# Optimization experiments

Measured on AMD Instinct MI355X. Metric: run time of the kernel, lower is better.

Reference implementation:

```python
import jax, jax.numpy as jnp
import numpy as np

N_RAYS = 131072
N_NODES = 524288
ENC_DEPTH = 8
ENC_DIM = 16
N_POINTS = 8
IN_DIM = N_POINTS * ENC_DEPTH * ENC_DIM  # 1024
INNER = 64


def setup_inputs() -> dict:
    key = jax.random.key(0)
    ks = jax.random.split(key, 9)
    orig = jax.random.uniform(ks[0], (N_RAYS, 3), dtype=jnp.float32)
    end = jax.random.uniform(ks[1], (N_RAYS, 3), dtype=jnp.float32)
    history = jax.random.randint(ks[2], (N_RAYS, ENC_DEPTH), 0, N_NODES, dtype=jnp.int32).astype(jnp.int64)
    nodes_min = jax.random.uniform(ks[3], (N_NODES, 3), dtype=jnp.float32)
    # extents strictly positive (module replaces 0 extents with 0.5)
    nodes_extent = jax.random.uniform(ks[4], (N_NODES, 3), dtype=jnp.float32) + 0.1
    emb = jax.random.normal(ks[5], (N_NODES, 8 * ENC_DIM), dtype=jnp.float32) * 0.1
    W1 = jax.random.normal(ks[6], (IN_DIM, INNER), dtype=jnp.float32) * (1.0 / np.sqrt(IN_DIM))
    W2 = jax.random.normal(ks[7], (INNER, INNER), dtype=jnp.float32) * (1.0 / np.sqrt(INNER))
    W3 = jax.random.normal(ks[8], (INNER, 2), dtype=jnp.float32) * (1.0 / np.sqrt(INNER))
    return {"orig": orig, "end": end, "history": history, "nodes_min": nodes_min,
            "nodes_extent": nodes_extent, "emb": emb, "W1": W1, "W2": W2, "W3": W3}


def _net_forward(orig, end, history, nodes_min, nodes_extent, emb, W1, W2, W3):
    n = orig.shape[0]
    d = history.shape[1]
    # gather per-ray, per-depth node data (irregular access)
    nmin = nodes_min[history]          # (n, d, 3)
    ext = nodes_extent[history]        # (n, d, 3)
    po = jnp.clip((orig[:, None, :] - nmin) / ext, 0.0, 1.0)  # (n, d, 3)
    pe = jnp.clip((end[:, None, :] - nmin) / ext, 0.0, 1.0)
    ts = jnp.linspace(0.0, 1.0, N_POINTS, dtype=orig.dtype)
    pts = po[:, :, None, :] + (pe - po)[:, :, None, :] * ts[None, None, :, None]  # (n, d, P, 3)
    xd, yd, zd = pts[..., 0], pts[..., 1], pts[..., 2]
    # corner weights in the same order as bbox_feature.chunk(8): 000,100,010,001,101,011,110,111
    w = jnp.stack([
        (1 - xd) * (1 - yd) * (1 - zd),
        xd * (1 - yd) * (1 - zd),
        (1 - xd) * yd * (1 - zd),
        (1 - xd) * (1 - yd) * zd,
        xd * (1 - yd) * zd,
        (1 - xd) * yd * zd,
        xd * yd * (1 - zd),
        xd * yd * zd,
    ], axis=-1)                                    # (n, d, P, 8)
    corners = emb[history].reshape(n, d, 8, ENC_DIM)  # (n, d, 8, F)
    feat = jnp.einsum('ndpk,ndkf->ndpf', w, corners)  # (n, d, P, F)
    feat = feat.reshape(n, d * N_POINTS * ENC_DIM)    # concat over depth
    h = jax.nn.relu(feat @ W1)
    h = jax.nn.relu(h @ W2)
    a = h @ W3                                        # (n, 2)
    lengths = jnp.linalg.norm(end - orig, axis=-1)
    pred_cls = a[:, 0]
    pred_dist = a[:, 1] * lengths
    return jnp.stack([pred_cls, pred_dist], axis=-1)  # (n, 2)


def reference(orig, end, history, nodes_min, nodes_extent, emb, W1, W2, W3):
    return _net_forward(orig, end, history, nodes_min, nodes_extent, emb, W1, W2, W3)
```

## Files before the change

### kernel.cpp

```cpp
#include <hip/hip_runtime.h>
#include <hip/hip_bf16.h>
#include <cstdint>

#define ENC_DEPTH 8
#define RAYS_PER_BLOCK 64
#define THREADS 512

typedef __attribute__((ext_vector_type(8))) short bf16x8;
typedef __attribute__((ext_vector_type(4))) float f32x4;

__device__ __forceinline__ unsigned short f2bf(float x) {
    union { float f; unsigned u; } v; v.f = x;
    unsigned r = v.u + 0x7fffu + ((v.u >> 16) & 1u);
    return (unsigned short)(r >> 16);
}
__device__ __forceinline__ float bf2f(unsigned short h) {
    union { unsigned u; float f; } v; v.u = ((unsigned)h) << 16;
    return v.f;
}
__device__ __forceinline__ float clamp01(float x) {
    return fminf(fmaxf(x, 0.0f), 1.0f);
}

__global__ __launch_bounds__(THREADS, 4) void nbvh_kernel(
    const float* __restrict__ orig, const float* __restrict__ endp,
    const int* __restrict__ hist, const float* __restrict__ nodes_min,
    const float* __restrict__ nodes_extent, const float* __restrict__ emb,
    const float* __restrict__ W1, const float* __restrict__ W2,
    const float* __restrict__ W3, float* __restrict__ out)
{
    __shared__ int hist_s[RAYS_PER_BLOCK * ENC_DEPTH];
    __shared__ float oe_s[RAYS_PER_BLOCK * 6];
    __shared__ __align__(16) unsigned short corners_s[RAYS_PER_BLOCK * 136];
    __shared__ __align__(16) unsigned short feat_s[RAYS_PER_BLOCK * 144];
    __shared__ __align__(16) unsigned short w1t_s[64 * 144];
    __shared__ float h1_s[RAYS_PER_BLOCK * 65];

    const int t = threadIdx.x;
    const int r0 = blockIdx.x * RAYS_PER_BLOCK;
    const int wave = t >> 6;
    const int lane = t & 63;

    hist_s[t] = hist[r0 * ENC_DEPTH + t];
    if (t < RAYS_PER_BLOCK * 3) {
        int ray = t / 3, c = t - ray * 3;
        oe_s[ray * 6 + c]     = orig[(r0 + ray) * 3 + c];
        oe_s[ray * 6 + 3 + c] = endp[(r0 + ray) * 3 + c];
    }

    f32x4 acc0 = {0.f, 0.f, 0.f, 0.f};
    f32x4 acc1 = {0.f, 0.f, 0.f, 0.f};
    const int m0 = (wave >> 1) * 16;
    const int n0 = (wave & 1) * 32;

    __syncthreads();

    for (int d = 0; d < ENC_DEPTH; ++d) {
        {
            int ray = t >> 3, k = t & 7;
            int node = hist_s[(ray << 3) + d];
            const float4* ep = (const float4*)(emb + ((size_t)node << 7) + (k << 4));
            float4 e0 = ep[0], e1 = ep[1], e2 = ep[2], e3 = ep[3];
            float e[16];
            e[0]=e0.x; e[1]=e0.y; e[2]=e0.z; e[3]=e0.w;
            e[4]=e1.x; e[5]=e1.y; e[6]=e1.z; e[7]=e1.w;
            e[8]=e2.x; e[9]=e2.y; e[10]=e2.z; e[11]=e2.w;
            e[12]=e3.x; e[13]=e3.y; e[14]=e3.z; e[15]=e3.w;
            unsigned short* cb = corners_s + ray * 136 + k;
            #pragma unroll
            for (int f = 0; f < 16; ++f) cb[f << 3] = f2bf(e[f]);
        }
        {
            int rl = t >> 2, cg = (t & 3) << 4;
            const float4* wp = (const float4*)(W1 + (size_t)(d * 128 + rl) * 64 + cg);
            float4 a0v = wp[0], a1v = wp[1], a2v = wp[2], a3v = wp[3];
            float a[16];
            a[0]=a0v.x; a[1]=a0v.y; a[2]=a0v.z; a[3]=a0v.w;
            a[4]=a1v.x; a[5]=a1v.y; a[6]=a1v.z; a[7]=a1v.w;
            a[8]=a2v.x; a[9]=a2v.y; a[10]=a2v.z; a[11]=a2v.w;
            a[12]=a3v.x; a[13]=a3v.y; a[14]=a3v.z; a[15]=a3v.w;
            unsigned short* wb = w1t_s + (size_t)cg * 144 + rl;
            #pragma unroll
            for (int i = 0; i < 16; ++i) wb[i * 144] = f2bf(a[i]);
        }
        __syncthreads();

        {
            int ray = t >> 3, p = t & 7;
            int node = hist_s[(ray << 3) + d];
            float nm0 = nodes_min[node * 3 + 0];
            float nm1 = nodes_min[node * 3 + 1];
            float nm2 = nodes_min[node * 3 + 2];
            float ex0 = nodes_extent[node * 3 + 0];
            float ex1 = nodes_extent[node * 3 + 1];
            float ex2 = nodes_extent[node * 3 + 2];
            const float* oe = oe_s + ray * 6;
            float po0 = clamp01((oe[0] - nm0) / ex0);
            float po1 = clamp01((oe[1] - nm1) / ex1);
            float po2 = clamp01((oe[2] - nm2) / ex2);
            float pe0 = clamp01((oe[3] - nm0) / ex0);
            float pe1 = clamp01((oe[4] - nm1) / ex1);
            float pe2 = clamp01((oe[5] - nm2) / ex2);
            float tt = (float)p * (1.0f / 7.0f);
            float x = po0 + (pe0 - po0) * tt;
            float y = po1 + (pe1 - po1) * tt;
            float z = po2 + (pe2 - po2) * tt;
            float ox = 1.f - x, oy = 1.f - y, oz = 1.f - z;
            float w[8];
            w[0] = ox * oy * oz;  w[1] = x * oy * oz;
            w[2] = ox * y * oz;   w[3] = ox * oy * z;
            w[4] = x * oy * z;    w[5] = ox * y * z;
            w[6] = x * y * oz;    w[7] = x * y * z;
            const unsigned short* cbase = corners_s + ray * 136;
            unsigned short* fb = feat_s + ray * 144 + (p << 4);
            #pragma unroll
            for (int f = 0; f < 16; ++f) {
                bf16x8 cv = *(const bf16x8*)(cbase + (f << 3));
                float acc = 0.f;
                #pragma unroll
                for (int k = 0; k < 8; ++k)
                    acc = fmaf(w[k], bf2f((unsigned short)cv[k]), acc);
                fb[f] = f2bf(acc);
            }
        }
        __syncthreads();

        {
            int q = lane >> 4, c = lane & 15;
            #pragma unroll
            for (int kk = 0; kk < 4; ++kk) {
                int koff = kk * 32 + q * 8;
                bf16x8 af = *(const bf16x8*)(feat_s + (m0 + c) * 144 + koff);
                bf16x8 b0 = *(const bf16x8*)(w1t_s + (n0 + c) * 144 + koff);
                bf16x8 b1 = *(const bf16x8*)(w1t_s + (n0 + 16 + c) * 144 + koff);
                acc0 = __builtin_amdgcn_mfma_f32_16x16x32_bf16(af, b0, acc0, 0, 0, 0);
                acc1 = __builtin_amdgcn_mfma_f32_16x16x32_bf16(af, b1, acc1, 0, 0, 0);
            }
        }
        __syncthreads();
    }

    {
        int colb = lane & 15, rq = (lane >> 4) << 2;
        #pragma unroll
        for (int r = 0; r < 4; ++r) {
            h1_s[(m0 + rq + r) * 65 + n0 + colb]      = fmaxf(acc0[r], 0.f);
            h1_s[(m0 + rq + r) * 65 + n0 + 16 + colb] = fmaxf(acc1[r], 0.f);
        }
    }
    __syncthreads();

    float* h2_s = (float*)corners_s;
    {
        int ray = t >> 3, jg = (t & 7) << 3;
        float s[8];
        #pragma unroll
        for (int j = 0; j < 8; ++j) s[j] = 0.f;
        const float* hrow = h1_s + ray * 65;
        #pragma unroll 8
        for (int i = 0; i < 64; ++i) {
            float hv = hrow[i];
            const float4* wr = (const float4*)(W2 + (i << 6) + jg);
            float4 wa = wr[0], wb = wr[1];
            s[0] = fmaf(hv, wa.x, s[0]); s[1] = fmaf(hv, wa.y, s[1]);
            s[2] = fmaf(hv, wa.z, s[2]); s[3] = fmaf(hv, wa.w, s[3]);
            s[4] = fmaf(hv, wb.x, s[4]); s[5] = fmaf(hv, wb.y, s[5]);
            s[6] = fmaf(hv, wb.z, s[6]); s[7] = fmaf(hv, wb.w, s[7]);
        }
        float* hb = h2_s + ray * 66 + jg;
        #pragma unroll
        for (int j = 0; j < 8; ++j) hb[j] = fmaxf(s[j], 0.f);
    }
    __syncthreads();

    if (t < 128) {
        int ray = t >> 1, c = t & 1;
        const float* hrow = h2_s + ray * 66;
        float a = 0.f;
        #pragma unroll 16
        for (int i = 0; i < 64; ++i) a = fmaf(hrow[i], W3[i * 2 + c], a);
        if (c) {
            const float* oe = oe_s + ray * 6;
            float dx = oe[3] - oe[0], dy = oe[4] - oe[1], dz = oe[5] - oe[2];
            a *= sqrtf(dx * dx + dy * dy + dz * dz);
        }
        out[((r0 + ray) << 1) + c] = a;
    }
}

extern "C" void kernel_launch(void* const* d_in, const int* in_sizes, int n_in,
                              void* d_out, int out_size, void* d_ws, size_t ws_size,
                              hipStream_t stream) {
    const float* orig = (const float*)d_in[0];
    const float* endp = (const float*)d_in[1];
    const int*   hist = (const int*)d_in[2];
    const float* nmin = (const float*)d_in[3];
    const float* next = (const float*)d_in[4];
    const float* emb  = (const float*)d_in[5];
    const float* W1   = (const float*)d_in[6];
    const float* W2   = (const float*)d_in[7];
    const float* W3   = (const float*)d_in[8];
    float* out = (float*)d_out;
    const int n_rays = in_sizes[0] / 3;
    dim3 grid(n_rays / RAYS_PER_BLOCK);
    nbvh_kernel<<<grid, THREADS, 0, stream>>>(orig, endp, hist, nmin, next,
                                              emb, W1, W2, W3, out);
}
```

Before: 536.7 us.

## Rewrite kernel with async double-buffered embedding loads and register-built MFMA fragments

After: 546.3 us. Within noise of the previous version (+1.8%).

```diff
diff --git a/kernel.cpp b/kernel.cpp
--- a/kernel.cpp
+++ b/kernel.cpp
@@ -1,10 +1,9 @@
 #include <hip/hip_runtime.h>
-#include <hip/hip_bf16.h>
 #include <cstdint>
 
 #define ENC_DEPTH 8
-#define RAYS_PER_BLOCK 64
-#define THREADS 512
+#define RAYS 64
+#define THREADS 256
 
 typedef __attribute__((ext_vector_type(8))) short bf16x8;
 typedef __attribute__((ext_vector_type(4))) float f32x4;
@@ -14,177 +13,206 @@
     unsigned r = v.u + 0x7fffu + ((v.u >> 16) & 1u);
     return (unsigned short)(r >> 16);
 }
-__device__ __forceinline__ float bf2f(unsigned short h) {
-    union { unsigned u; float f; } v; v.u = ((unsigned)h) << 16;
-    return v.f;
-}
 __device__ __forceinline__ float clamp01(float x) {
     return fminf(fmaxf(x, 0.0f), 1.0f);
 }
-
-__global__ __launch_bounds__(THREADS, 4) void nbvh_kernel(
+__device__ __forceinline__ void async_copy16(const float* g, void* l) {
+    __builtin_amdgcn_global_load_lds(
+        (const __attribute__((address_space(1))) void*)g,
+        (__attribute__((address_space(3))) void*)l, 16, 0, 0);
+}
+
+__global__ void w1_frag_kernel(const float* __restrict__ W1,
+                               unsigned short* __restrict__ W1F) {
+    int slot = blockIdx.x * 256 + threadIdx.x;
+    int lane = slot & 63, tile = (slot >> 6) & 3, kk = (slot >> 8) & 3, d = slot >> 10;
+    int n = tile * 16 + (lane & 15);
+    int kbase = d * 128 + kk * 32 + (lane >> 4) * 8;
+    bf16x8 v;
+    #pragma unroll
+    for (int j = 0; j < 8; ++j) v[j] = (short)f2bf(W1[(size_t)(kbase + j) * 64 + n]);
+    *(bf16x8*)(W1F + (size_t)slot * 8) = v;
+}
+
+__global__ __launch_bounds__(THREADS) void nbvh2(
     const float* __restrict__ orig, const float* __restrict__ endp,
     const int* __restrict__ hist, const float* __restrict__ nodes_min,
     const float* __restrict__ nodes_extent, const float* __restrict__ emb,
-    const float* __restrict__ W1, const float* __restrict__ W2,
+    const unsigned short* __restrict__ W1F, const float* __restrict__ W2,
     const float* __restrict__ W3, float* __restrict__ out)
 {
-    __shared__ int hist_s[RAYS_PER_BLOCK * ENC_DEPTH];
-    __shared__ float oe_s[RAYS_PER_BLOCK * 6];
-    __shared__ __align__(16) unsigned short corners_s[RAYS_PER_BLOCK * 136];
-    __shared__ __align__(16) unsigned short feat_s[RAYS_PER_BLOCK * 144];
-    __shared__ __align__(16) unsigned short w1t_s[64 * 144];
-    __shared__ float h1_s[RAYS_PER_BLOCK * 65];
+    __shared__ __align__(16) float cbuf[2][8320];
+    __shared__ float pope_s[RAYS * ENC_DEPTH * 6];
+    __shared__ int hist_s[RAYS * ENC_DEPTH];
 
     const int t = threadIdx.x;
-    const int r0 = blockIdx.x * RAYS_PER_BLOCK;
-    const int wave = t >> 6;
-    const int lane = t & 63;
+    const int lane = t & 63, w = t >> 6;
+    const int r0 = blockIdx.x * RAYS;
 
     hist_s[t] = hist[r0 * ENC_DEPTH + t];
-    if (t < RAYS_PER_BLOCK * 3) {
-        int ray = t / 3, c = t - ray * 3;
-        oe_s[ray * 6 + c]     = orig[(r0 + ray) * 3 + c];
-        oe_s[ray * 6 + 3 + c] = endp[(r0 + ray) * 3 + c];
-    }
-
-    f32x4 acc0 = {0.f, 0.f, 0.f, 0.f};
-    f32x4 acc1 = {0.f, 0.f, 0.f, 0.f};
-    const int m0 = (wave >> 1) * 16;
-    const int n0 = (wave & 1) * 32;
-
-    __syncthreads();
-
+    hist_s[t + 256] = hist[r0 * ENC_DEPTH + t + 256];
+    __syncthreads();
+
+    {
+        #pragma unroll
+        for (int r = 0; r < 8; ++r) {
+            int ray = r * 8 + w * 2 + (lane >> 5);
+            int node = hist_s[(ray << 3) + 0];
+            const float* g = emb + ((size_t)node << 7) + ((lane & 31) << 2);
+            char* l = (char*)(&cbuf[0][0]) + (r * 4 + w) * 1040 + lane * 16;
+            async_copy16(g, l);
+        }
+    }
+
+    #pragma unroll
+    for (int rep = 0; rep < 2; ++rep) {
+        int task = t + rep * 256;
+        int ray = task >> 3;
+        int node = hist_s[task];
+        float nm0 = nodes_min[node * 3 + 0], nm1 = nodes_min[node * 3 + 1], nm2 = nodes_min[node * 3 + 2];
+        float ex0 = nodes_extent[node * 3 + 0], ex1 = nodes_extent[node * 3 + 1], ex2 = nodes_extent[node * 3 + 2];
+        float o0 = orig[(r0 + ray) * 3 + 0], o1 = orig[(r0 + ray) * 3 + 1], o2 = orig[(r0 + ray) * 3 + 2];
+        float e0 = endp[(r0 + ray) * 3 + 0], e1 = endp[(r0 + ray) * 3 + 1], e2 = endp[(r0 + ray) * 3 + 2];
+        float* pp = pope_s + task * 6;
+        pp[0] = clamp01((o0 - nm0) / ex0);
+        pp[1] = clamp01((o1 - nm1) / ex1);
+        pp[2] = clamp01((o2 - nm2) / ex2);
+        pp[3] = clamp01((e0 - nm0) / ex0);
+        pp[4] = clamp01((e1 - nm1) / ex1);
+        pp[5] = clamp01((e2 - nm2) / ex2);
+    }
+    __syncthreads();
+
+    f32x4 acc[4];
+    #pragma unroll
+    for (int i = 0; i < 4; ++i) acc[i] = (f32x4){0.f, 0.f, 0.f, 0.f};
+
+    const int c = lane & 15, q = lane >> 4;
+    const int ray = w * 16 + c;
+    const int qh = q & 1;
+    const int qp = q >> 1;
+
+    #pragma unroll 1
     for (int d = 0; d < ENC_DEPTH; ++d) {
-        {
-            int ray = t >> 3, k = t & 7;
-            int node = hist_s[(ray << 3) + d];
-            const float4* ep = (const float4*)(emb + ((size_t)node << 7) + (k << 4));
-            float4 e0 = ep[0], e1 = ep[1], e2 = ep[2], e3 = ep[3];
-            float e[16];
-            e[0]=e0.x; e[1]=e0.y; e[2]=e0.z; e[3]=e0.w;
-            e[4]=e1.x; e[5]=e1.y; e[6]=e1.z; e[7]=e1.w;
-            e[8]=e2.x; e[9]=e2.y; e[10]=e2.z; e[11]=e2.w;
-            e[12]=e3.x; e[13]=e3.y; e[14]=e3.z; e[15]=e3.w;
-            unsigned short* cb = corners_s + ray * 136 + k;
-            #pragma unroll
-            for (int f = 0; f < 16; ++f) cb[f << 3] = f2bf(e[f]);
-        }
-        {
-            int rl = t >> 2, cg = (t & 3) << 4;
-            const float4* wp = (const float4*)(W1 + (size_t)(d * 128 + rl) * 64 + cg);
-            float4 a0v = wp[0], a1v = wp[1], a2v = wp[2], a3v = wp[3];
-            float a[16];
-            a[0]=a0v.x; a[1]=a0v.y; a[2]=a0v.z; a[3]=a0v.w;
-            a[4]=a1v.x; a[5]=a1v.y; a[6]=a1v.z; a[7]=a1v.w;
-            a[8]=a2v.x; a[9]=a2v.y; a[10]=a2v.z; a[11]=a2v.w;
-            a[12]=a3v.x; a[13]=a3v.y; a[14]=a3v.z; a[15]=a3v.w;
-            unsigned short* wb = w1t_s + (size_t)cg * 144 + rl;
-            #pragma unroll
-            for (int i = 0; i < 16; ++i) wb[i * 144] = f2bf(a[i]);
+        if (d < ENC_DEPTH - 1) {
+            float* dst = &cbuf[(d + 1) & 1][0];
+            #pragma unroll
+            for (int r = 0; r < 8; ++r) {
+                int rr = r * 8 + w * 2 + (lane >> 5);
+                int node = hist_s[(rr << 3) + d + 1];
+                const float* g = emb + ((size_t)node << 7) + ((lane & 31) << 2);
+                char* l = (char*)dst + (r * 4 + w) * 1040 + lane * 16;
+                async_copy16(g, l);
+            }
+        }
+
+        bf16x8 bfr[4][4];
+        #pragma unroll
+        for (int kk = 0; kk < 4; ++kk)
+            #pragma unroll
+            for (int tile = 0; tile < 4; ++tile)
+                bfr[kk][tile] = *(const bf16x8*)(W1F +
+                    ((size_t)(((d * 4 + kk) * 4 + tile) * 64 + lane)) * 8);
+
+        const float* pp = pope_s + ((ray << 3) + d) * 6;
+        float po0 = pp[0], po1 = pp[1], po2 = pp[2], pe0 = pp[3], pe1 = pp[4], pe2 = pp[5];
+        float X[4], OX[4], Y[4], OY[4], Z[4], OZ[4];
+        #pragma unroll
+        for (int kk = 0; kk < 4; ++kk) {
+            float tp = (float)(2 * kk + qp) * (1.0f / 7.0f);
+            X[kk] = po0 + (pe0 - po0) * tp; OX[kk] = 1.f - X[kk];
+            Y[kk] = po1 + (pe1 - po1) * tp; OY[kk] = 1.f - Y[kk];
+            Z[kk] = po2 + (pe2 - po2) * tp; OZ[kk] = 1.f - Z[kk];
+        }
+
+        float fa[4][8];
+        #pragma unroll
+        for (int kk = 0; kk < 4; ++kk)
+            #pragma unroll
+            for (int j = 0; j < 8; ++j) fa[kk][j] = 0.f;
+
+        const float* crow = &cbuf[d & 1][0] + (ray >> 1) * 260 + (ray & 1) * 128 + (qh << 3);
+        #pragma unroll
+        for (int c8 = 0; c8 < 8; ++c8) {
+            float4 ea = *(const float4*)(crow + c8 * 16);
+            float4 eb = *(const float4*)(crow + c8 * 16 + 4);
+            #pragma unroll
+            for (int kk = 0; kk < 4; ++kk) {
+                float wx = ((0xD2 >> c8) & 1) ? X[kk] : OX[kk];
+                float wy = ((0xE4 >> c8) & 1) ? Y[kk] : OY[kk];
+                float wz = ((0xB8 >> c8) & 1) ? Z[kk] : OZ[kk];
+                float wgt = wx * wy * wz;
+                fa[kk][0] = fmaf(wgt, ea.x, fa[kk][0]);
+                fa[kk][1] = fmaf(wgt, ea.y, fa[kk][1]);
+                fa[kk][2] = fmaf(wgt, ea.z, fa[kk][2]);
+                fa[kk][3] = fmaf(wgt, ea.w, fa[kk][3]);
+                fa[kk][4] = fmaf(wgt, eb.x, fa[kk][4]);
+                fa[kk][5] = fmaf(wgt, eb.y, fa[kk][5]);
+                fa[kk][6] = fmaf(wgt, eb.z, fa[kk][6]);
+                fa[kk][7] = fmaf(wgt, eb.w, fa[kk][7]);
+            }
+        }
+
+        #pragma unroll
+        for (int kk = 0; kk < 4; ++kk) {
+            bf16x8 af;
+            #pragma unroll
+            for (int j = 0; j < 8; ++j) af[j] = (short)f2bf(fa[kk][j]);
+            #pragma unroll
+            for (int tile = 0; tile < 4; ++tile)
+                acc[tile] = __builtin_amdgcn_mfma_f32_16x16x32_bf16(af, bfr[kk][tile], acc[tile], 0, 0, 0);
         }
         __syncthreads();
-
-        {
-            int ray = t >> 3, p = t & 7;
-            int node = hist_s[(ray << 3) + d];
-            float nm0 = nodes_min[node * 3 + 0];
-            float nm1 = nodes_min[node * 3 + 1];
-            float nm2 = nodes_min[node * 3 + 2];
-            float ex0 = nodes_extent[node * 3 + 0];
-            float ex1 = nodes_extent[node * 3 + 1];
-            float ex2 = nodes_extent[node * 3 + 2];
-            const float* oe = oe_s + ray * 6;
-            float po0 = clamp01((oe[0] - nm0) / ex0);
-            float po1 = clamp01((oe[1] - nm1) / ex1);
-            float po2 = clamp01((oe[2] - nm2) / ex2);
-            float pe0 = clamp01((oe[3] - nm0) / ex0);
-            float pe1 = clamp01((oe[4] - nm1) / ex1);
-            float pe2 = clamp01((oe[5] - nm2) / ex2);
-            float tt = (float)p * (1.0f / 7.0f);
-            float x = po0 + (pe0 - po0) * tt;
-            float y = po1 + (pe1 - po1) * tt;
-            float z = po2 + (pe2 - po2) * tt;
-            float ox = 1.f - x, oy = 1.f - y, oz = 1.f - z;
-            float w[8];
-            w[0] = ox * oy * oz;  w[1] = x * oy * oz;
-            w[2] = ox * y * oz;   w[3] = ox * oy * z;
-            w[4] = x * oy * z;    w[5] = ox * y * z;
-            w[6] = x * y * oz;    w[7] = x * y * z;
-            const unsigned short* cbase = corners_s + ray * 136;
-            unsigned short* fb = feat_s + ray * 144 + (p << 4);
-            #pragma unroll
-            for (int f = 0; f < 16; ++f) {
-                bf16x8 cv = *(const bf16x8*)(cbase + (f << 3));
-                float acc = 0.f;
-                #pragma unroll
-                for (int k = 0; k < 8; ++k)
-                    acc = fmaf(w[k], bf2f((unsigned short)cv[k]), acc);
-                fb[f] = f2bf(acc);
-            }
-        }
-        __syncthreads();
-
-        {
-            int q = lane >> 4, c = lane & 15;
-            #pragma unroll
-            for (int kk = 0; kk < 4; ++kk) {
-                int koff = kk * 32 + q * 8;
-                bf16x8 af = *(const bf16x8*)(feat_s + (m0 + c) * 144 + koff);
-                bf16x8 b0 = *(const bf16x8*)(w1t_s + (n0 + c) * 144 + koff);
-                bf16x8 b1 = *(const bf16x8*)(w1t_s + (n0 + 16 + c) * 144 + koff);
-                acc0 = __builtin_amdgcn_mfma_f32_16x16x32_bf16(af, b0, acc0, 0, 0, 0);
-                acc1 = __builtin_amdgcn_mfma_f32_16x16x32_bf16(af, b1, acc1, 0, 0, 0);
-            }
-        }
-        __syncthreads();
-    }
-
+    }
+
+    float* h1 = &cbuf[0][0];
+    #pragma unroll
+    for (int tile = 0; tile < 4; ++tile)
+        #pragma unroll
+        for (int r = 0; r < 4; ++r)
+            h1[(w * 16 + q * 4 + r) * 68 + tile * 16 + c] = fmaxf(acc[tile][r], 0.f);
+    __syncthreads();
+
+    float* h2 = &cbuf[1][0];
     {
-        int colb = lane & 15, rq = (lane >> 4) << 2;
-        #pragma unroll
-        for (int r = 0; r < 4; ++r) {
-            h1_s[(m0 + rq + r) * 65 + n0 + colb]      = fmaxf(acc0[r], 0.f);
-            h1_s[(m0 + rq + r) * 65 + n0 + 16 + colb] = fmaxf(acc1[r], 0.f);
-        }
-    }
-    __syncthreads();
-
-    float* h2_s = (float*)corners_s;
-    {
-        int ray = t >> 3, jg = (t & 7) << 3;
-        float s[8];
-        #pragma unroll
-        for (int j = 0; j < 8; ++j) s[j] = 0.f;
-        const float* hrow = h1_s + ray * 65;
-        #pragma unroll 8
+        int ray2 = t >> 2, jg = (t & 3) << 4;
+        float s[16];
+        #pragma unroll
+        for (int j = 0; j < 16; ++j) s[j] = 0.f;
+        const float* hrow = h1 + ray2 * 68;
+        #pragma unroll 4
         for (int i = 0; i < 64; ++i) {
             float hv = hrow[i];
             const float4* wr = (const float4*)(W2 + (i << 6) + jg);
-            float4 wa = wr[0], wb = wr[1];
-            s[0] = fmaf(hv, wa.x, s[0]); s[1] = fmaf(hv, wa.y, s[1]);
-            s[2] = fmaf(hv, wa.z, s[2]); s[3] = fmaf(hv, wa.w, s[3]);
-            s[4] = fmaf(hv, wb.x, s[4]); s[5] = fmaf(hv, wb.y, s[5]);
-            s[6] = fmaf(hv, wb.z, s[6]); s[7] = fmaf(hv, wb.w, s[7]);
-        }
-        float* hb = h2_s + ray * 66 + jg;
-        #pragma unroll
-        for (int j = 0; j < 8; ++j) hb[j] = fmaxf(s[j], 0.f);
+            float4 a0 = wr[0], a1 = wr[1], a2 = wr[2], a3 = wr[3];
+            s[0]  = fmaf(hv, a0.x, s[0]);  s[1]  = fmaf(hv, a0.y, s[1]);
+            s[2]  = fmaf(hv, a0.z, s[2]);  s[3]  = fmaf(hv, a0.w, s[3]);
+            s[4]  = fmaf(hv, a1.x, s[4]);  s[5]  = fmaf(hv, a1.y, s[5]);
+            s[6]  = fmaf(hv, a1.z, s[6]);  s[7]  = fmaf(hv, a1.w, s[7]);
+            s[8]  = fmaf(hv, a2.x, s[8]);  s[9]  = fmaf(hv, a2.y, s[9]);
+            s[10] = fmaf(hv, a2.z, s[10]); s[11] = fmaf(hv, a2.w, s[11]);
+            s[12] = fmaf(hv, a3.x, s[12]); s[13] = fmaf(hv, a3.y, s[13]);
+            s[14] = fmaf(hv, a3.z, s[14]); s[15] = fmaf(hv, a3.w, s[15]);
+        }
+        float* h2row = h2 + ray2 * 68 + jg;
+        #pragma unroll
+        for (int j = 0; j < 16; ++j) h2row[j] = fmaxf(s[j], 0.f);
     }
     __syncthreads();
 
     if (t < 128) {
-        int ray = t >> 1, c = t & 1;
-        const float* hrow = h2_s + ray * 66;
+        int ray3 = t >> 1, cc = t & 1;
+        const float* hrow = h2 + ray3 * 68;
         float a = 0.f;
         #pragma unroll 16
-        for (int i = 0; i < 64; ++i) a = fmaf(hrow[i], W3[i * 2 + c], a);
-        if (c) {
-            const float* oe = oe_s + ray * 6;
-            float dx = oe[3] - oe[0], dy = oe[4] - oe[1], dz = oe[5] - oe[2];
+        for (int i = 0; i < 64; ++i) a = fmaf(hrow[i], W3[i * 2 + cc], a);
+        if (cc) {
+            float dx = endp[(r0 + ray3) * 3 + 0] - orig[(r0 + ray3) * 3 + 0];
+            float dy = endp[(r0 + ray3) * 3 + 1] - orig[(r0 + ray3) * 3 + 1];
+            float dz = endp[(r0 + ray3) * 3 + 2] - orig[(r0 + ray3) * 3 + 2];
             a *= sqrtf(dx * dx + dy * dy + dz * dz);
         }
-        out[((r0 + ray) << 1) + c] = a;
+        out[((r0 + ray3) << 1) + cc] = a;
     }
 }
 
@@ -201,8 +229,11 @@
     const float* W2   = (const float*)d_in[7];
     const float* W3   = (const float*)d_in[8];
     float* out = (float*)d_out;
+    unsigned short* W1F = (unsigned short*)d_ws;
+
+    w1_frag_kernel<<<dim3(32), dim3(256), 0, stream>>>(W1, W1F);
+
     const int n_rays = in_sizes[0] / 3;
-    dim3 grid(n_rays / RAYS_PER_BLOCK);
-    nbvh_kernel<<<grid, THREADS, 0, stream>>>(orig, endp, hist, nmin, next,
-                                              emb, W1, W2, W3, out);
-}
+    nbvh2<<<dim3(n_rays / RAYS), dim3(THREADS), 0, stream>>>(
+        orig, endp, hist, nmin, next, emb, W1F, W2, W3, out);
+}
```
